# Kernel optimization log

Hardware: AMD Instinct MI355X
Metric: run time of the kernel (lower is better)

The kernel has to match this reference:

```python
import jax, jax.numpy as jnp
import numpy as np

HEAD, STACK = 8, 2
EPS = 1e-5


def _ln2d(x):
    # F.layer_norm(x, x.size()[1:]): normalize over (seq, feature) jointly, no affine
    m = jnp.mean(x, axis=(1, 2), keepdims=True)
    v = jnp.var(x, axis=(1, 2), keepdims=True)
    return (x - m) / jnp.sqrt(v + EPS)


def setup_inputs() -> dict:
    key = jax.random.key(0)
    ks = jax.random.split(key, 8)
    B, S, V, E, D, C = 64, 1024, 8000, 200, 200, 31
    g = lambda k, shape, sc: (jax.random.normal(k, shape, jnp.float32) * sc)
    return dict(
        x=jax.random.randint(ks[0], (B, S), 0, V),
        embed=g(ks[1], (V, E), 0.02),
        pos=g(ks[2], (S, E), 0.02),
        Wp=g(ks[3], (E, D), 0.05), bp=jnp.zeros((D,), jnp.float32),
        Wm=g(ks[4], (D * HEAD, D), 0.05), bm=jnp.zeros((D,), jnp.float32),
        W1=g(ks[5], (D, D), 0.05), b1=jnp.zeros((D,), jnp.float32),
        W2=g(ks[6], (D, D), 0.05), b2=jnp.zeros((D,), jnp.float32),
        Wd=g(ks[7], (D, C), 0.05), bd=jnp.zeros((C,), jnp.float32),
    )


def reference(x, embed, pos, Wp, bp, Wm, bm, W1, b1, W2, b2, Wd, bd):
    h = embed[x] + pos                       # [B,S,200]
    scale = jnp.sqrt(jnp.asarray(Wp.shape[1], jnp.float32))
    for _ in range(STACK):                   # weights shared across stacks (aliased in torch)
        r = h
        p = h @ Wp + bp                      # q = k = v (same aliased Linear in torch)
        a = jax.nn.softmax(jnp.einsum('bsd,btd->bst', p, p) / scale, axis=-1)
        c = jnp.einsum('bst,btd->bsd', a, p)  # [B,S,200]
        cat = jnp.tile(c, (1, 1, HEAD))       # all heads identical -> concat = tile
        h = _ln2d(cat @ Wm + bm + r)
        r = h
        ff = jax.nn.relu(h @ W1 + b1) @ W2 + b2
        h = _ln2d(ff + r)
    return h[:, -1, :] @ Wd + bd             # [B, class_num]; dropout = identity (eval)
```

## Files before the change

### kernel.cpp

```cpp
#include <hip/hip_runtime.h>
#include <cstddef>
#include <cstdint>
#include <cmath>

#define BDIM  64
#define SDIM  1024
#define DDIM  200
#define DPAD  224
#define WROWS 256
#define PSTRIDE 232
#define CDIM  31
#define NSTACK 2
#define EPS   1e-5f
#define LN_N  204800.0f
#define PREP_BLOCKS 224

typedef __attribute__((ext_vector_type(8))) short short8;
typedef __attribute__((ext_vector_type(4))) short short4_t;
typedef __attribute__((ext_vector_type(4))) float f32x4;

__device__ __forceinline__ short f2bf(float f) {
    union { float f; unsigned u; } v; v.f = f;
    unsigned r = v.u + 0x7FFFu + ((v.u >> 16) & 1u);
    return (short)(r >> 16);
}
__device__ __forceinline__ float bf2f(short s) {
    union { unsigned u; float f; } v; v.u = ((unsigned)(unsigned short)s) << 16;
    return v.f;
}
__device__ __forceinline__ unsigned cvtpk_bf16(float a, float b) {
    unsigned r;
    asm volatile("v_cvt_pk_bf16_f32 %0, %1, %2" : "=v"(r) : "v"(a), "v"(b));
    return r;
}
__device__ __forceinline__ void gload_lds16(const short* g, short* l) {
    __builtin_amdgcn_global_load_lds(
        (const __attribute__((address_space(1))) void*)g,
        (__attribute__((address_space(3))) void*)l, 16, 0, 0);
}

__global__ void prep_embed_kernel(const int* __restrict__ x, const float* __restrict__ embed,
                                  const float* __restrict__ pos,
                                  const float* __restrict__ Wp, const float* __restrict__ bp,
                                  const float* __restrict__ Wm, const float* __restrict__ bm,
                                  const float* __restrict__ W1, const float* __restrict__ b1,
                                  const float* __restrict__ W2, const float* __restrict__ b2,
                                  short* __restrict__ WtP, short* __restrict__ WtM,
                                  short* __restrict__ Wt1, short* __restrict__ Wt2,
                                  float* __restrict__ bpP, float* __restrict__ bmP,
                                  float* __restrict__ b1P, float* __restrict__ b2P,
                                  float* __restrict__ csP, float* __restrict__ cs1,
                                  short* __restrict__ h, float* __restrict__ parts)
{
    if (blockIdx.x < PREP_BLOCKS) {
        int idx = blockIdx.x * 256 + threadIdx.x;
        if (idx >= WROWS * DPAD) return;
        int n = idx / DPAD, k = idx - n * DPAD;
        bool valid = (n < DDIM) && (k < DDIM);
        WtP[idx] = valid ? f2bf(Wp[(size_t)k * DDIM + n]) : 0;
        Wt1[idx] = valid ? f2bf(W1[(size_t)k * DDIM + n]) : 0;
        Wt2[idx] = valid ? f2bf(W2[(size_t)k * DDIM + n]) : 0;
        float s = 0.f;
        if (valid) {
            #pragma unroll
            for (int blk = 0; blk < 8; ++blk)
                s += Wm[(size_t)(blk * DDIM + k) * DDIM + n];
        }
        WtM[idx] = valid ? f2bf(s) : 0;
        if (idx < DPAD) {
            bpP[idx] = idx < DDIM ? bp[idx] : 0.f;
            bmP[idx] = idx < DDIM ? bm[idx] : 0.f;
            b1P[idx] = idx < DDIM ? b1[idx] : 0.f;
            b2P[idx] = idx < DDIM ? b2[idx] : 0.f;
            float sp = 0.f, s1 = 0.f;
            if (idx < DDIM) {
                for (int kk = 0; kk < DDIM; ++kk) {
                    sp += bf2f(f2bf(Wp[(size_t)kk * DDIM + idx]));
                    s1 += bf2f(f2bf(W1[(size_t)kk * DDIM + idx]));
                }
            }
            csP[idx] = sp;
            cs1[idx] = s1;
        }
        return;
    }

    const int eb = blockIdx.x - PREP_BLOCKS;
    if (eb == 0) {
        for (int i = threadIdx.x; i < 4 * BDIM * 2; i += 256) parts[i] = 0.f;
    }
    const int total = BDIM * SDIM * (DPAD / 4);
    for (int i = eb * 256 + threadIdx.x; i < total; i += 2048 * 256) {
        const int row = i / (DPAD / 4);
        const int n0  = (i - row * (DPAD / 4)) * 4;
        short4_t o;
        if (n0 >= DDIM) {
            o[0] = o[1] = o[2] = o[3] = 0;
        } else {
            const int s = row & (SDIM - 1);
            const int tok = x[row];
            const float4 e  = *(const float4*)(embed + (size_t)tok * DDIM + n0);
            const float4 p4 = *(const float4*)(pos + (size_t)s * DDIM + n0);
            o[0] = f2bf(e.x + p4.x); o[1] = f2bf(e.y + p4.y);
            o[2] = f2bf(e.z + p4.z); o[3] = f2bf(e.w + p4.w);
        }
        *(short4_t*)(h + (size_t)row * DPAD + n0) = o;
    }
}

#define WSLICE 8192
__global__ __launch_bounds__(256, 3)
void gemm_bf(const short* __restrict__ act, const float* __restrict__ actParts,
             const short* __restrict__ Wt, const float* __restrict__ bias,
             const float* __restrict__ csW,
             const short* __restrict__ res, const float* __restrict__ resParts,
             short* __restrict__ out, short* __restrict__ pt,
             float* __restrict__ parts, int doRelu, int outStride)
{
    __shared__ short WB[3][WSLICE];

    const int tid  = threadIdx.x;
    const int wave = tid >> 6, lane = tid & 63;
    const int lo   = lane & 15, hi = lane >> 4;
    const int mblk = blockIdx.x * 128;
    const int m0   = mblk + wave * 32;

    auto stage = [&](int ks, int buf) {
        #pragma unroll
        for (int cc = 0; cc < 4; ++cc) {
            int c = wave + cc * 4;
            int row = c * 16 + (lane >> 2);
            int kc  = (lane & 3) ^ ((row >> 1) & 3);
            gload_lds16(Wt + (size_t)row * DPAD + ks * 32 + kc * 8,
                        &WB[buf][c * 512 + lane * 8]);
        }
    };

    f32x4 acc[2][14];
    #pragma unroll
    for (int mt = 0; mt < 2; ++mt)
        #pragma unroll
        for (int nt = 0; nt < 14; ++nt) acc[mt][nt] = (f32x4){0.f, 0.f, 0.f, 0.f};

    short8 af[2], afn[2];
    #pragma unroll
    for (int mt = 0; mt < 2; ++mt)
        af[mt] = *(const short8*)(act + (size_t)(m0 + mt * 16 + lo) * DPAD + hi * 8);
    stage(0, 0);
    stage(1, 1);
    asm volatile("s_waitcnt vmcnt(4)" ::: "memory");
    __builtin_amdgcn_s_barrier();

    #pragma unroll
    for (int ks = 0; ks < 7; ++ks) {
        const int cur = ks % 3;
        if (ks < 6) {
            #pragma unroll
            for (int mt = 0; mt < 2; ++mt)
                afn[mt] = *(const short8*)(act + (size_t)(m0 + mt * 16 + lo) * DPAD
                                           + (ks + 1) * 32 + hi * 8);
        }
        if (ks < 5) stage(ks + 2, (ks + 2) % 3);

        #pragma unroll
        for (int nt = 0; nt < 14; ++nt) {
            int brow = nt * 16 + lo;
            short8 bf_ = *(const short8*)&WB[cur][brow * 32
                                                  + ((hi * 8) ^ (((brow >> 1) & 3) << 3))];
            acc[0][nt] = __builtin_amdgcn_mfma_f32_16x16x32_bf16(af[0], bf_, acc[0][nt], 0, 0, 0);
            acc[1][nt] = __builtin_amdgcn_mfma_f32_16x16x32_bf16(af[1], bf_, acc[1][nt], 0, 0, 0);
        }

        if (ks < 5) {
            asm volatile("s_waitcnt vmcnt(6)" ::: "memory");
            __builtin_amdgcn_s_barrier();
        } else if (ks == 5) {
            asm volatile("s_waitcnt vmcnt(2)" ::: "memory");
            __builtin_amdgcn_s_barrier();
        }
        if (ks < 6) { af[0] = afn[0]; af[1] = afn[1]; }
    }

    const int bb = mblk >> 10;
    float inv_a = 1.f, corr = 0.f;
    if (actParts) {
        float mean = actParts[bb * 2] / LN_N;
        inv_a = rsqrtf(actParts[bb * 2 + 1] / LN_N - mean * mean + EPS);
        corr = mean * inv_a;
    }
    float mean_r = 0.f, inv_r = 1.f;
    if (resParts) {
        mean_r = resParts[bb * 2] / LN_N;
        inv_r = rsqrtf(resParts[bb * 2 + 1] / LN_N - mean_r * mean_r + EPS);
    }

    float s = 0.f, s2 = 0.f;
    #pragma unroll
    for (int mt = 0; mt < 2; ++mt) {
        #pragma unroll
        for (int nt = 0; nt < 14; ++nt) {
            const int n = nt * 16 + lo;
            const float bn = bias[n];
            const float cw = actParts ? csW[n] : 0.f;
            float v[4];
            #pragma unroll
            for (int r = 0; r < 4; ++r)
                v[r] = acc[mt][nt][r] * inv_a + bn - corr * cw;
            if (res) {
                #pragma unroll
                for (int r = 0; r < 4; ++r) {
                    int m = m0 + mt * 16 + hi * 4 + r;
                    v[r] += (bf2f(res[(size_t)m * DPAD + n]) - mean_r) * inv_r;
                }
            }
            if (doRelu)
                #pragma unroll
                for (int r = 0; r < 4; ++r) v[r] = fmaxf(v[r], 0.f);
            if (n >= DDIM)
                #pragma unroll
                for (int r = 0; r < 4; ++r) v[r] = 0.f;
            if (parts)
                #pragma unroll
                for (int r = 0; r < 4; ++r) { s += v[r]; s2 = fmaf(v[r], v[r], s2); }
            short4_t o4;
            #pragma unroll
            for (int r = 0; r < 4; ++r) o4[r] = f2bf(v[r]);
            #pragma unroll
            for (int r = 0; r < 4; ++r) {
                int m = m0 + mt * 16 + hi * 4 + r;
                out[(size_t)m * outStride + n] = o4[r];
            }
            if (pt && nt < 13) {
                const int sloc = (m0 + mt * 16 + hi * 4) & (SDIM - 1);
                *(short4_t*)(pt + ((size_t)bb * DPAD + n) * SDIM + sloc) = o4;
            }
        }
    }

    if (parts) {
        __shared__ float rs[4], rq[4];
        #pragma unroll
        for (int off = 32; off; off >>= 1) {
            s  += __shfl_down(s, off);
            s2 += __shfl_down(s2, off);
        }
        if (lane == 0) { rs[wave] = s; rq[wave] = s2; }
        __syncthreads();
        if (tid == 0) {
            atomicAdd(&parts[bb * 2],     rs[0] + rs[1] + rs[2] + rs[3]);
            atomicAdd(&parts[bb * 2 + 1], rq[0] + rq[1] + rq[2] + rq[3]);
        }
    }
}

#define Y1S 232
__global__ __launch_bounds__(256, 2)
void ffn_bf(const short* __restrict__ act, const float* __restrict__ actParts,
            const float* __restrict__ csW1,
            const short* __restrict__ Wt1, const float* __restrict__ b1,
            const short* __restrict__ Wt2, const float* __restrict__ b2,
            short* __restrict__ out, float* __restrict__ parts)
{
    __shared__ short WB[3][WSLICE];
    __shared__ short Y1[64 * Y1S];

    const int tid  = threadIdx.x;
    const int wave = tid >> 6, lane = tid & 63;
    const int lo   = lane & 15, hi = lane >> 4;
    const int mblk = blockIdx.x * 64;
    const int m0   = mblk + wave * 16;
    const int bb   = mblk >> 10;

    auto stageJ = [&](int j) {
        const short* W = (j < 7) ? Wt1 : Wt2;
        const int kk = (j < 7) ? j : j - 7;
        const int buf = j % 3;
        #pragma unroll
        for (int cc = 0; cc < 4; ++cc) {
            int c = wave + cc * 4;
            int row = c * 16 + (lane >> 2);
            int kc  = (lane & 3) ^ ((row >> 1) & 3);
            gload_lds16(W + (size_t)row * DPAD + kk * 32 + kc * 8,
                        &WB[buf][c * 512 + lane * 8]);
        }
    };

    const float mean_a = actParts[bb * 2] / LN_N;
    const float inv_a  = rsqrtf(actParts[bb * 2 + 1] / LN_N - mean_a * mean_a + EPS);
    const float corr   = mean_a * inv_a;

    f32x4 acc[14];
    #pragma unroll
    for (int nt = 0; nt < 14; ++nt) acc[nt] = (f32x4){0.f, 0.f, 0.f, 0.f};

    short8 af = *(const short8*)(act + (size_t)(m0 + lo) * DPAD + hi * 8);
    short8 afn;
    stageJ(0);
    stageJ(1);
    asm volatile("s_waitcnt vmcnt(4)" ::: "memory");
    __builtin_amdgcn_s_barrier();

    #pragma unroll
    for (int ks = 0; ks < 7; ++ks) {
        const int cur = ks % 3;
        if (ks < 6)
            afn = *(const short8*)(act + (size_t)(m0 + lo) * DPAD + (ks + 1) * 32 + hi * 8);
        stageJ(ks + 2);
        #pragma unroll
        for (int nt = 0; nt < 14; ++nt) {
            int brow = nt * 16 + lo;
            short8 bf_ = *(const short8*)&WB[cur][brow * 32
                                                  + ((hi * 8) ^ (((brow >> 1) & 3) << 3))];
            acc[nt] = __builtin_amdgcn_mfma_f32_16x16x32_bf16(af, bf_, acc[nt], 0, 0, 0);
        }
        if (ks < 6) {
            asm volatile("s_waitcnt vmcnt(5)" ::: "memory");
            __builtin_amdgcn_s_barrier();
            af = afn;
        }
    }

    #pragma unroll
    for (int nt = 0; nt < 14; ++nt) {
        const int n = nt * 16 + lo;
        const float bn = b1[n];
        const float cw = csW1[n];
        #pragma unroll
        for (int r = 0; r < 4; ++r) {
            float v = fmaxf(acc[nt][r] * inv_a + bn - corr * cw, 0.f);
            Y1[(wave * 16 + hi * 4 + r) * Y1S + n] = f2bf(v);
        }
    }
    __syncthreads();

    #pragma unroll
    for (int nt = 0; nt < 14; ++nt) acc[nt] = (f32x4){0.f, 0.f, 0.f, 0.f};

    #pragma unroll
    for (int j = 7; j < 14; ++j) {
        const int cur = j % 3;
        if (j < 12) stageJ(j + 2);
        short8 a2 = *(const short8*)&Y1[(wave * 16 + lo) * Y1S + (j - 7) * 32 + hi * 8];
        #pragma unroll
        for (int nt = 0; nt < 14; ++nt) {
            int brow = nt * 16 + lo;
            short8 bf_ = *(const short8*)&WB[cur][brow * 32
                                                  + ((hi * 8) ^ (((brow >> 1) & 3) << 3))];
            acc[nt] = __builtin_amdgcn_mfma_f32_16x16x32_bf16(a2, bf_, acc[nt], 0, 0, 0);
        }
        if (j < 12)       asm volatile("s_waitcnt vmcnt(4)" ::: "memory");
        else if (j == 12) asm volatile("s_waitcnt vmcnt(0)" ::: "memory");
        if (j < 13) __builtin_amdgcn_s_barrier();
    }

    float s = 0.f, s2 = 0.f;
    #pragma unroll
    for (int nt = 0; nt < 14; ++nt) {
        const int n = nt * 16 + lo;
        const float bn = b2[n];
        float v[4];
        #pragma unroll
        for (int r = 0; r < 4; ++r) {
            int m = m0 + hi * 4 + r;
            v[r] = acc[nt][r] + bn + (bf2f(act[(size_t)m * DPAD + n]) - mean_a) * inv_a;
        }
        if (n >= DDIM)
            #pragma unroll
            for (int r = 0; r < 4; ++r) v[r] = 0.f;
        #pragma unroll
        for (int r = 0; r < 4; ++r) { s += v[r]; s2 = fmaf(v[r], v[r], s2); }
        #pragma unroll
        for (int r = 0; r < 4; ++r) {
            int m = m0 + hi * 4 + r;
            out[(size_t)m * DPAD + n] = f2bf(v[r]);
        }
    }

    {
        __shared__ float rs[4], rq[4];
        #pragma unroll
        for (int off = 32; off; off >>= 1) {
            s  += __shfl_down(s, off);
            s2 += __shfl_down(s2, off);
        }
        if (lane == 0) { rs[wave] = s; rq[wave] = s2; }
        __syncthreads();
        if (tid == 0) {
            atomicAdd(&parts[bb * 2],     rs[0] + rs[1] + rs[2] + rs[3]);
            atomicAdd(&parts[bb * 2 + 1], rq[0] + rq[1] + rq[2] + rq[3]);
        }
    }
}

__global__ __launch_bounds__(256, 2)
void attn_kernel(const short* __restrict__ pbf, const short* __restrict__ pt,
                 short* __restrict__ c, float qscale)
{
    __shared__ short Kbuf[2][7680];
    __shared__ short Vbuf[2][6656];

    const int bid = blockIdx.x;
    const int wg  = (bid & 7) * 64 + (bid >> 3);
    const int b   = wg >> 3;
    const int q0  = (wg & 7) * 128;

    const int tid  = threadIdx.x;
    const int wave = tid >> 6;
    const int lane = tid & 63;
    const int lo   = lane & 15;
    const int hi   = lane >> 4;

    const short* pb  = pbf + (size_t)b * SDIM * PSTRIDE;
    const short* ptb = pt  + (size_t)b * DPAD * SDIM;

    auto stage = [&](int kt2, int bufIdx) {
        const short* ks = pb + (size_t)kt2 * 32 * PSTRIDE + lane * 8;
        #pragma unroll
        for (int i = 0; i < 15; ++i)
            gload_lds16(ks + i * 512, &Kbuf[bufIdx][i * 512]);
        #pragma unroll
        for (int i = 0; i < 13; ++i) {
            int e = i * 512 + lane * 8;
            int d = e >> 5;
            int cc = (e & 31) ^ (((d >> 1) & 3) << 3);
            gload_lds16(ptb + (size_t)d * SDIM + kt2 * 32 + cc, &Vbuf[bufIdx][i * 512]);
        }
    };

    short8 qf[2][7];
    #pragma unroll
    for (int qt = 0; qt < 2; ++qt)
        #pragma unroll
        for (int ks = 0; ks < 7; ++ks) {
            short8 q = *(const short8*)(pb + (size_t)(q0 + wave * 32 + qt * 16 + lo) * PSTRIDE
                                        + ks * 32 + hi * 8);
            short8 qs;
            #pragma unroll
            for (int j = 0; j < 8; ++j) qs[j] = f2bf(bf2f(q[j]) * qscale);
            qf[qt][ks] = qs;
        }

    f32x4 o[2][13];
    float m[2], ell[2];
    #pragma unroll
    for (int qt = 0; qt < 2; ++qt) {
        #pragma unroll
        for (int n = 0; n < 13; ++n) o[qt][n] = (f32x4){0.f, 0.f, 0.f, 0.f};
        m[qt] = -1e30f; ell[qt] = 0.f;
    }

    if (wave == 0) stage(0, 0);
    __syncthreads();

    for (int kt = 0; kt < 32; ++kt) {
        const int cur = kt & 1;
        if (kt < 31 && wave == ((kt + 1) & 3)) stage(kt + 1, cur ^ 1);

        f32x4 sacc[2][2];
        #pragma unroll
        for (int qt = 0; qt < 2; ++qt)
            #pragma unroll
            for (int t = 0; t < 2; ++t) sacc[qt][t] = (f32x4){0.f, 0.f, 0.f, 0.f};
        __builtin_amdgcn_s_setprio(1);
        #pragma unroll
        for (int t = 0; t < 2; ++t)
            #pragma unroll
            for (int ks = 0; ks < 7; ++ks) {
                short8 kf = *(const short8*)(&Kbuf[cur][(t * 16 + lo) * PSTRIDE + ks * 32 + hi * 8]);
                sacc[0][t] = __builtin_amdgcn_mfma_f32_16x16x32_bf16(kf, qf[0][ks], sacc[0][t], 0, 0, 0);
                sacc[1][t] = __builtin_amdgcn_mfma_f32_16x16x32_bf16(kf, qf[1][ks], sacc[1][t], 0, 0, 0);
            }
        __builtin_amdgcn_s_setprio(0);

        short8 pa[2];
        #pragma unroll
        for (int qt = 0; qt < 2; ++qt) {
            float mx = fmaxf(fmaxf(fmaxf(sacc[qt][0][0], sacc[qt][0][1]),
                                   fmaxf(sacc[qt][0][2], sacc[qt][0][3])),
                             fmaxf(fmaxf(sacc[qt][1][0], sacc[qt][1][1]),
                                   fmaxf(sacc[qt][1][2], sacc[qt][1][3])));
            mx = fmaxf(mx, __shfl_xor(mx, 16));
            mx = fmaxf(mx, __shfl_xor(mx, 32));
            if (__any(mx > m[qt] + 11.5f)) {
                float mn = fmaxf(m[qt], mx);
                float al = exp2f(m[qt] - mn);
                m[qt] = mn; ell[qt] *= al;
                float alr[4];
                #pragma unroll
                for (int r = 0; r < 4; ++r) alr[r] = __shfl(al, hi * 4 + r);
                #pragma unroll
                for (int n = 0; n < 13; ++n)
                    #pragma unroll
                    for (int r = 0; r < 4; ++r) o[qt][n][r] *= alr[r];
            }
            float p[2][4]; float rsum = 0.f;
            #pragma unroll
            for (int t = 0; t < 2; ++t)
                #pragma unroll
                for (int r = 0; r < 4; ++r) {
                    p[t][r] = exp2f(sacc[qt][t][r] - m[qt]);
                    rsum += p[t][r];
                }
            rsum += __shfl_xor(rsum, 16);
            rsum += __shfl_xor(rsum, 32);
            ell[qt] += rsum;
            unsigned pk01_0 = cvtpk_bf16(p[0][0], p[0][1]);
            unsigned pk23_0 = cvtpk_bf16(p[0][2], p[0][3]);
            unsigned pk01_1 = cvtpk_bf16(p[1][0], p[1][1]);
            unsigned pk23_1 = cvtpk_bf16(p[1][2], p[1][3]);
            const int srcA = lo + ((hi & 1) * 2) * 16;
            const int srcB = srcA + 16;
            int a0 = __shfl((int)pk01_0, srcA), a1 = __shfl((int)pk01_1, srcA);
            int b0 = __shfl((int)pk23_0, srcA), b1 = __shfl((int)pk23_1, srcA);
            int c0 = __shfl((int)pk01_0, srcB), c1 = __shfl((int)pk01_1, srcB);
            int d0 = __shfl((int)pk23_0, srcB), d1 = __shfl((int)pk23_1, srcB);
            const bool thi = (hi >> 1) != 0;
            union { short8 s; int u[4]; } pu;
            pu.u[0] = thi ? a1 : a0;
            pu.u[1] = thi ? b1 : b0;
            pu.u[2] = thi ? c1 : c0;
            pu.u[3] = thi ? d1 : d0;
            pa[qt] = pu.s;
        }

        __builtin_amdgcn_s_setprio(1);
        #pragma unroll
        for (int n = 0; n < 13; ++n) {
            int d = n * 16 + lo;
            int addr = d * 32 + ((hi * 8) ^ (((d >> 1) & 3) << 3));
            short8 vf = *(const short8*)(&Vbuf[cur][addr]);
            o[0][n] = __builtin_amdgcn_mfma_f32_16x16x32_bf16(pa[0], vf, o[0][n], 0, 0, 0);
            o[1][n] = __builtin_amdgcn_mfma_f32_16x16x32_bf16(pa[1], vf, o[1][n], 0, 0, 0);
        }
        __builtin_amdgcn_s_setprio(0);

        __syncthreads();
    }

    #pragma unroll
    for (int qt = 0; qt < 2; ++qt) {
        float inv_l = 1.f / ell[qt];
        float invr[4];
        #pragma unroll
        for (int r = 0; r < 4; ++r) invr[r] = __shfl(inv_l, hi * 4 + r);
        #pragma unroll
        for (int n = 0; n < 13; ++n) {
            int dcol = n * 16 + lo;
            #pragma unroll
            for (int r = 0; r < 4; ++r) {
                size_t row = (size_t)b * SDIM + q0 + wave * 32 + qt * 16 + hi * 4 + r;
                c[row * DPAD + dcol] = f2bf(o[qt][n][r] * invr[r]);
            }
        }
        #pragma unroll
        for (int r = 0; r < 4; ++r) {
            size_t row = (size_t)b * SDIM + q0 + wave * 32 + qt * 16 + hi * 4 + r;
            c[row * DPAD + 208 + lo] = 0;
        }
    }
}

__global__ void final_kernel(const short* __restrict__ y, const float* __restrict__ parts,
                             const float* __restrict__ Wd, const float* __restrict__ bd,
                             float* __restrict__ out)
{
    const int b = blockIdx.x;
    const float sum = parts[b * 2], sq = parts[b * 2 + 1];
    const float mean = sum / LN_N;
    const float inv  = rsqrtf(sq / LN_N - mean * mean + EPS);
    __shared__ float hrow[DDIM];
    const short* row = y + ((size_t)b * SDIM + SDIM - 1) * DPAD;
    for (int d = threadIdx.x; d < DDIM; d += blockDim.x)
        hrow[d] = (bf2f(row[d]) - mean) * inv;
    __syncthreads();
    if (threadIdx.x < CDIM) {
        float acc = bd[threadIdx.x];
        for (int d = 0; d < DDIM; ++d)
            acc = fmaf(hrow[d], Wd[(size_t)d * CDIM + threadIdx.x], acc);
        out[(size_t)b * CDIM + threadIdx.x] = acc;
    }
}

extern "C" void kernel_launch(void* const* d_in, const int* in_sizes, int n_in,
                              void* d_out, int out_size, void* d_ws, size_t ws_size,
                              hipStream_t stream)
{
    const int*   x     = (const int*)  d_in[0];
    const float* embed = (const float*)d_in[1];
    const float* pos   = (const float*)d_in[2];
    const float* Wp    = (const float*)d_in[3];
    const float* bp    = (const float*)d_in[4];
    const float* Wm    = (const float*)d_in[5];
    const float* bm    = (const float*)d_in[6];
    const float* W1    = (const float*)d_in[7];
    const float* b1    = (const float*)d_in[8];
    const float* W2    = (const float*)d_in[9];
    const float* b2    = (const float*)d_in[10];
    const float* Wd    = (const float*)d_in[11];
    const float* bd    = (const float*)d_in[12];
    float* out = (float*)d_out;

    const size_t HB = (size_t)BDIM * SDIM * DPAD;
    const size_t PB = (size_t)BDIM * SDIM * PSTRIDE;
    const size_t WTSZ = (size_t)WROWS * DPAD;

    short* h_bf  = (short*)d_ws;
    short* p_bf  = h_bf  + HB;
    short* pt    = p_bf  + PB;
    short* cb_bf = pt    + HB;
    short* yA    = cb_bf + HB;
    short* yB    = yA    + HB;
    short* WtP   = yB + HB;
    short* WtM   = WtP + WTSZ;
    short* Wt1   = WtM + WTSZ;
    short* Wt2   = Wt1 + WTSZ;
    float* bpP   = (float*)(Wt2 + WTSZ);
    float* bmP   = bpP + DPAD;
    float* b1P   = bmP + DPAD;
    float* b2P   = b1P + DPAD;
    float* csP   = b2P + DPAD;
    float* cs1   = csP + DPAD;
    float* parts = cs1 + DPAD;
    const size_t need = (size_t)((char*)(parts + 4 * BDIM * 2) - (char*)d_ws);
    if (ws_size < need) return;

    float* pA1 = parts;
    float* pB1 = parts + BDIM * 2;
    float* pA2 = parts + 2 * BDIM * 2;
    float* pB2 = parts + 3 * BDIM * 2;

    prep_embed_kernel<<<dim3(PREP_BLOCKS + 2048), dim3(256), 0, stream>>>(
        x, embed, pos, Wp, bp, Wm, bm, W1, b1, W2, b2,
        WtP, WtM, Wt1, Wt2, bpP, bmP, b1P, b2P, csP, cs1, h_bf, parts);

    const float qscale = 1.44269504f / sqrtf((float)DDIM);

    gemm_bf<<<dim3(512), dim3(256), 0, stream>>>(h_bf, nullptr, WtP, bpP, nullptr,
                                                 nullptr, nullptr, p_bf, pt, nullptr, 0, PSTRIDE);
    attn_kernel<<<dim3(512), dim3(256), 0, stream>>>(p_bf, pt, cb_bf, qscale);
    gemm_bf<<<dim3(512), dim3(256), 0, stream>>>(cb_bf, nullptr, WtM, bmP, nullptr,
                                                 h_bf, nullptr, yA, nullptr, pA1, 0, DPAD);
    ffn_bf<<<dim3(1024), dim3(256), 0, stream>>>(yA, pA1, cs1, Wt1, b1P, Wt2, b2P, yB, pB1);
    gemm_bf<<<dim3(512), dim3(256), 0, stream>>>(yB, pB1, WtP, bpP, csP,
                                                 nullptr, nullptr, p_bf, pt, nullptr, 0, PSTRIDE);
    attn_kernel<<<dim3(512), dim3(256), 0, stream>>>(p_bf, pt, cb_bf, qscale);
    gemm_bf<<<dim3(512), dim3(256), 0, stream>>>(cb_bf, nullptr, WtM, bmP, nullptr,
                                                 yB, pB1, h_bf, nullptr, pA2, 0, DPAD);
    ffn_bf<<<dim3(1024), dim3(256), 0, stream>>>(h_bf, pA2, cs1, Wt1, b1P, Wt2, b2P, yA, pB2);
    final_kernel<<<dim3(BDIM), dim3(64), 0, stream>>>(yA, pB2, Wd, bd, out);
}
```

Baseline: 380.3 us.

## Fuse attention with the merge-projection GEMM into one kernel

Attention and the following Wm projection GEMM (with residual, layernorm statistics and atomics) now run in one kernel. Each block writes its attention output rows to global memory, then reuses the same shared memory for triple-buffered Wm slices and runs the GEMM on the rows it just produced. This removes two kernel launches and the separate pass that re-read the attention output. The cost is larger register and LDS pressure in the fused kernel, and the attention output is still written to global memory and read back through cache.

```diff
diff --git a/kernel.cpp b/kernel.cpp
--- a/kernel.cpp
+++ b/kernel.cpp
@@ -14,6 +14,7 @@
 #define EPS   1e-5f
 #define LN_N  204800.0f
 #define PREP_BLOCKS 224
+#define WSLICE 8192
 
 typedef __attribute__((ext_vector_type(8))) short short8;
 typedef __attribute__((ext_vector_type(4))) short short4_t;
@@ -108,14 +109,11 @@
     }
 }
 
-#define WSLICE 8192
 __global__ __launch_bounds__(256, 3)
 void gemm_bf(const short* __restrict__ act, const float* __restrict__ actParts,
              const short* __restrict__ Wt, const float* __restrict__ bias,
              const float* __restrict__ csW,
-             const short* __restrict__ res, const float* __restrict__ resParts,
-             short* __restrict__ out, short* __restrict__ pt,
-             float* __restrict__ parts, int doRelu, int outStride)
+             short* __restrict__ out, short* __restrict__ pt, int outStride)
 {
     __shared__ short WB[3][WSLICE];
 
@@ -188,13 +186,7 @@
         inv_a = rsqrtf(actParts[bb * 2 + 1] / LN_N - mean * mean + EPS);
         corr = mean * inv_a;
     }
-    float mean_r = 0.f, inv_r = 1.f;
-    if (resParts) {
-        mean_r = resParts[bb * 2] / LN_N;
-        inv_r = rsqrtf(resParts[bb * 2 + 1] / LN_N - mean_r * mean_r + EPS);
-    }
-
-    float s = 0.f, s2 = 0.f;
+
     #pragma unroll
     for (int mt = 0; mt < 2; ++mt) {
         #pragma unroll
@@ -206,22 +198,9 @@
             #pragma unroll
             for (int r = 0; r < 4; ++r)
                 v[r] = acc[mt][nt][r] * inv_a + bn - corr * cw;
-            if (res) {
-                #pragma unroll
-                for (int r = 0; r < 4; ++r) {
-                    int m = m0 + mt * 16 + hi * 4 + r;
-                    v[r] += (bf2f(res[(size_t)m * DPAD + n]) - mean_r) * inv_r;
-                }
-            }
-            if (doRelu)
-                #pragma unroll
-                for (int r = 0; r < 4; ++r) v[r] = fmaxf(v[r], 0.f);
             if (n >= DDIM)
                 #pragma unroll
                 for (int r = 0; r < 4; ++r) v[r] = 0.f;
-            if (parts)
-                #pragma unroll
-                for (int r = 0; r < 4; ++r) { s += v[r]; s2 = fmaf(v[r], v[r], s2); }
             short4_t o4;
             #pragma unroll
             for (int r = 0; r < 4; ++r) o4[r] = f2bf(v[r]);
@@ -230,174 +209,27 @@
                 int m = m0 + mt * 16 + hi * 4 + r;
                 out[(size_t)m * outStride + n] = o4[r];
             }
-            if (pt && nt < 13) {
+            if (nt < 13) {
                 const int sloc = (m0 + mt * 16 + hi * 4) & (SDIM - 1);
                 *(short4_t*)(pt + ((size_t)bb * DPAD + n) * SDIM + sloc) = o4;
             }
         }
     }
-
-    if (parts) {
-        __shared__ float rs[4], rq[4];
-        #pragma unroll
-        for (int off = 32; off; off >>= 1) {
-            s  += __shfl_down(s, off);
-            s2 += __shfl_down(s2, off);
-        }
-        if (lane == 0) { rs[wave] = s; rq[wave] = s2; }
-        __syncthreads();
-        if (tid == 0) {
-            atomicAdd(&parts[bb * 2],     rs[0] + rs[1] + rs[2] + rs[3]);
-            atomicAdd(&parts[bb * 2 + 1], rq[0] + rq[1] + rq[2] + rq[3]);
-        }
-    }
-}
-
-#define Y1S 232
+}
+
 __global__ __launch_bounds__(256, 2)
-void ffn_bf(const short* __restrict__ act, const float* __restrict__ actParts,
-            const float* __restrict__ csW1,
-            const short* __restrict__ Wt1, const float* __restrict__ b1,
-            const short* __restrict__ Wt2, const float* __restrict__ b2,
-            short* __restrict__ out, float* __restrict__ parts)
+void attn_gemm2(const short* __restrict__ pbf, const short* __restrict__ pt,
+                const short* __restrict__ WtM, const float* __restrict__ bias,
+                const short* __restrict__ res, const float* __restrict__ resParts,
+                short* __restrict__ cb, short* __restrict__ out,
+                float* __restrict__ parts, float qscale)
 {
-    __shared__ short WB[3][WSLICE];
-    __shared__ short Y1[64 * Y1S];
-
-    const int tid  = threadIdx.x;
-    const int wave = tid >> 6, lane = tid & 63;
-    const int lo   = lane & 15, hi = lane >> 4;
-    const int mblk = blockIdx.x * 64;
-    const int m0   = mblk + wave * 16;
-    const int bb   = mblk >> 10;
-
-    auto stageJ = [&](int j) {
-        const short* W = (j < 7) ? Wt1 : Wt2;
-        const int kk = (j < 7) ? j : j - 7;
-        const int buf = j % 3;
-        #pragma unroll
-        for (int cc = 0; cc < 4; ++cc) {
-            int c = wave + cc * 4;
-            int row = c * 16 + (lane >> 2);
-            int kc  = (lane & 3) ^ ((row >> 1) & 3);
-            gload_lds16(W + (size_t)row * DPAD + kk * 32 + kc * 8,
-                        &WB[buf][c * 512 + lane * 8]);
-        }
-    };
-
-    const float mean_a = actParts[bb * 2] / LN_N;
-    const float inv_a  = rsqrtf(actParts[bb * 2 + 1] / LN_N - mean_a * mean_a + EPS);
-    const float corr   = mean_a * inv_a;
-
-    f32x4 acc[14];
-    #pragma unroll
-    for (int nt = 0; nt < 14; ++nt) acc[nt] = (f32x4){0.f, 0.f, 0.f, 0.f};
-
-    short8 af = *(const short8*)(act + (size_t)(m0 + lo) * DPAD + hi * 8);
-    short8 afn;
-    stageJ(0);
-    stageJ(1);
-    asm volatile("s_waitcnt vmcnt(4)" ::: "memory");
-    __builtin_amdgcn_s_barrier();
-
-    #pragma unroll
-    for (int ks = 0; ks < 7; ++ks) {
-        const int cur = ks % 3;
-        if (ks < 6)
-            afn = *(const short8*)(act + (size_t)(m0 + lo) * DPAD + (ks + 1) * 32 + hi * 8);
-        stageJ(ks + 2);
-        #pragma unroll
-        for (int nt = 0; nt < 14; ++nt) {
-            int brow = nt * 16 + lo;
-            short8 bf_ = *(const short8*)&WB[cur][brow * 32
-                                                  + ((hi * 8) ^ (((brow >> 1) & 3) << 3))];
-            acc[nt] = __builtin_amdgcn_mfma_f32_16x16x32_bf16(af, bf_, acc[nt], 0, 0, 0);
-        }
-        if (ks < 6) {
-            asm volatile("s_waitcnt vmcnt(5)" ::: "memory");
-            __builtin_amdgcn_s_barrier();
-            af = afn;
-        }
-    }
-
-    #pragma unroll
-    for (int nt = 0; nt < 14; ++nt) {
-        const int n = nt * 16 + lo;
-        const float bn = b1[n];
-        const float cw = csW1[n];
-        #pragma unroll
-        for (int r = 0; r < 4; ++r) {
-            float v = fmaxf(acc[nt][r] * inv_a + bn - corr * cw, 0.f);
-            Y1[(wave * 16 + hi * 4 + r) * Y1S + n] = f2bf(v);
-        }
-    }
-    __syncthreads();
-
-    #pragma unroll
-    for (int nt = 0; nt < 14; ++nt) acc[nt] = (f32x4){0.f, 0.f, 0.f, 0.f};
-
-    #pragma unroll
-    for (int j = 7; j < 14; ++j) {
-        const int cur = j % 3;
-        if (j < 12) stageJ(j + 2);
-        short8 a2 = *(const short8*)&Y1[(wave * 16 + lo) * Y1S + (j - 7) * 32 + hi * 8];
-        #pragma unroll
-        for (int nt = 0; nt < 14; ++nt) {
-            int brow = nt * 16 + lo;
-            short8 bf_ = *(const short8*)&WB[cur][brow * 32
-                                                  + ((hi * 8) ^ (((brow >> 1) & 3) << 3))];
-            acc[nt] = __builtin_amdgcn_mfma_f32_16x16x32_bf16(a2, bf_, acc[nt], 0, 0, 0);
-        }
-        if (j < 12)       asm volatile("s_waitcnt vmcnt(4)" ::: "memory");
-        else if (j == 12) asm volatile("s_waitcnt vmcnt(0)" ::: "memory");
-        if (j < 13) __builtin_amdgcn_s_barrier();
-    }
-
-    float s = 0.f, s2 = 0.f;
-    #pragma unroll
-    for (int nt = 0; nt < 14; ++nt) {
-        const int n = nt * 16 + lo;
-        const float bn = b2[n];
-        float v[4];
-        #pragma unroll
-        for (int r = 0; r < 4; ++r) {
-            int m = m0 + hi * 4 + r;
-            v[r] = acc[nt][r] + bn + (bf2f(act[(size_t)m * DPAD + n]) - mean_a) * inv_a;
-        }
-        if (n >= DDIM)
-            #pragma unroll
-            for (int r = 0; r < 4; ++r) v[r] = 0.f;
-        #pragma unroll
-        for (int r = 0; r < 4; ++r) { s += v[r]; s2 = fmaf(v[r], v[r], s2); }
-        #pragma unroll
-        for (int r = 0; r < 4; ++r) {
-            int m = m0 + hi * 4 + r;
-            out[(size_t)m * DPAD + n] = f2bf(v[r]);
-        }
-    }
-
-    {
-        __shared__ float rs[4], rq[4];
-        #pragma unroll
-        for (int off = 32; off; off >>= 1) {
-            s  += __shfl_down(s, off);
-            s2 += __shfl_down(s2, off);
-        }
-        if (lane == 0) { rs[wave] = s; rq[wave] = s2; }
-        __syncthreads();
-        if (tid == 0) {
-            atomicAdd(&parts[bb * 2],     rs[0] + rs[1] + rs[2] + rs[3]);
-            atomicAdd(&parts[bb * 2 + 1], rq[0] + rq[1] + rq[2] + rq[3]);
-        }
-    }
-}
-
-__global__ __launch_bounds__(256, 2)
-void attn_kernel(const short* __restrict__ pbf, const short* __restrict__ pt,
-                 short* __restrict__ c, float qscale)
-{
-    __shared__ short Kbuf[2][7680];
-    __shared__ short Vbuf[2][6656];
+    __shared__ short SH[28672];
+
+    short* Kb0 = SH;
+    short* Kb1 = SH + 7680;
+    short* Vb0 = SH + 15360;
+    short* Vb1 = SH + 22016;
 
     const int bid = blockIdx.x;
     const int wg  = (bid & 7) * 64 + (bid >> 3);
@@ -413,17 +245,19 @@
     const short* pb  = pbf + (size_t)b * SDIM * PSTRIDE;
     const short* ptb = pt  + (size_t)b * DPAD * SDIM;
 
-    auto stage = [&](int kt2, int bufIdx) {
+    auto stageKV = [&](int kt2, int bufIdx) {
+        short* kb = bufIdx ? Kb1 : Kb0;
+        short* vb = bufIdx ? Vb1 : Vb0;
         const short* ks = pb + (size_t)kt2 * 32 * PSTRIDE + lane * 8;
         #pragma unroll
         for (int i = 0; i < 15; ++i)
-            gload_lds16(ks + i * 512, &Kbuf[bufIdx][i * 512]);
+            gload_lds16(ks + i * 512, kb + i * 512);
         #pragma unroll
         for (int i = 0; i < 13; ++i) {
             int e = i * 512 + lane * 8;
             int d = e >> 5;
             int cc = (e & 31) ^ (((d >> 1) & 3) << 3);
-            gload_lds16(ptb + (size_t)d * SDIM + kt2 * 32 + cc, &Vbuf[bufIdx][i * 512]);
+            gload_lds16(ptb + (size_t)d * SDIM + kt2 * 32 + cc, vb + i * 512);
         }
     };
 
@@ -449,12 +283,14 @@
         m[qt] = -1e30f; ell[qt] = 0.f;
     }
 
-    if (wave == 0) stage(0, 0);
+    if (wave == 0) stageKV(0, 0);
     __syncthreads();
 
     for (int kt = 0; kt < 32; ++kt) {
         const int cur = kt & 1;
-        if (kt < 31 && wave == ((kt + 1) & 3)) stage(kt + 1, cur ^ 1);
+        if (kt < 31 && wave == ((kt + 1) & 3)) stageKV(kt + 1, cur ^ 1);
+        const short* kb = cur ? Kb1 : Kb0;
+        const short* vb = cur ? Vb1 : Vb0;
 
         f32x4 sacc[2][2];
         #pragma unroll
@@ -466,7 +302,7 @@
         for (int t = 0; t < 2; ++t)
             #pragma unroll
             for (int ks = 0; ks < 7; ++ks) {
-                short8 kf = *(const short8*)(&Kbuf[cur][(t * 16 + lo) * PSTRIDE + ks * 32 + hi * 8]);
+                short8 kf = *(const short8*)(kb + (t * 16 + lo) * PSTRIDE + ks * 32 + hi * 8);
                 sacc[0][t] = __builtin_amdgcn_mfma_f32_16x16x32_bf16(kf, qf[0][ks], sacc[0][t], 0, 0, 0);
                 sacc[1][t] = __builtin_amdgcn_mfma_f32_16x16x32_bf16(kf, qf[1][ks], sacc[1][t], 0, 0, 0);
             }
@@ -528,7 +364,7 @@
         for (int n = 0; n < 13; ++n) {
             int d = n * 16 + lo;
             int addr = d * 32 + ((hi * 8) ^ (((d >> 1) & 3) << 3));
-            short8 vf = *(const short8*)(&Vbuf[cur][addr]);
+            short8 vf = *(const short8*)(vb + addr);
             o[0][n] = __builtin_amdgcn_mfma_f32_16x16x32_bf16(pa[0], vf, o[0][n], 0, 0, 0);
             o[1][n] = __builtin_amdgcn_mfma_f32_16x16x32_bf16(pa[1], vf, o[1][n], 0, 0, 0);
         }
@@ -549,13 +385,266 @@
             #pragma unroll
             for (int r = 0; r < 4; ++r) {
                 size_t row = (size_t)b * SDIM + q0 + wave * 32 + qt * 16 + hi * 4 + r;
-                c[row * DPAD + dcol] = f2bf(o[qt][n][r] * invr[r]);
+                cb[row * DPAD + dcol] = f2bf(o[qt][n][r] * invr[r]);
             }
         }
         #pragma unroll
         for (int r = 0; r < 4; ++r) {
             size_t row = (size_t)b * SDIM + q0 + wave * 32 + qt * 16 + hi * 4 + r;
-            c[row * DPAD + 208 + lo] = 0;
+            cb[row * DPAD + 208 + lo] = 0;
+        }
+    }
+    asm volatile("s_waitcnt vmcnt(0)" ::: "memory");
+    __builtin_amdgcn_s_barrier();
+
+    short* WB0 = SH;
+    short* WB1 = SH + WSLICE;
+    short* WB2 = SH + 2 * WSLICE;
+
+    const int m0 = b * SDIM + q0 + wave * 32;
+
+    auto stageW = [&](int ks, int buf) {
+        short* wb = (buf == 0) ? WB0 : (buf == 1) ? WB1 : WB2;
+        #pragma unroll
+        for (int cc = 0; cc < 4; ++cc) {
+            int c = wave + cc * 4;
+            int row = c * 16 + (lane >> 2);
+            int kc  = (lane & 3) ^ ((row >> 1) & 3);
+            gload_lds16(WtM + (size_t)row * DPAD + ks * 32 + kc * 8,
+                        wb + c * 512 + lane * 8);
+        }
+    };
+
+    f32x4 acc[2][14];
+    #pragma unroll
+    for (int mt = 0; mt < 2; ++mt)
+        #pragma unroll
+        for (int nt = 0; nt < 14; ++nt) acc[mt][nt] = (f32x4){0.f, 0.f, 0.f, 0.f};
+
+    short8 af[2], afn[2];
+    #pragma unroll
+    for (int mt = 0; mt < 2; ++mt)
+        af[mt] = *(const short8*)(cb + (size_t)(m0 + mt * 16 + lo) * DPAD + hi * 8);
+    stageW(0, 0);
+    stageW(1, 1);
+    asm volatile("s_waitcnt vmcnt(4)" ::: "memory");
+    __builtin_amdgcn_s_barrier();
+
+    #pragma unroll
+    for (int ks = 0; ks < 7; ++ks) {
+        const int cur = ks % 3;
+        short* wb = (cur == 0) ? WB0 : (cur == 1) ? WB1 : WB2;
+        if (ks < 6) {
+            #pragma unroll
+            for (int mt = 0; mt < 2; ++mt)
+                afn[mt] = *(const short8*)(cb + (size_t)(m0 + mt * 16 + lo) * DPAD
+                                           + (ks + 1) * 32 + hi * 8);
+        }
+        if (ks < 5) stageW(ks + 2, (ks + 2) % 3);
+
+        #pragma unroll
+        for (int nt = 0; nt < 14; ++nt) {
+            int brow = nt * 16 + lo;
+            short8 bf_ = *(const short8*)&wb[brow * 32
+                                             + ((hi * 8) ^ (((brow >> 1) & 3) << 3))];
+            acc[0][nt] = __builtin_amdgcn_mfma_f32_16x16x32_bf16(af[0], bf_, acc[0][nt], 0, 0, 0);
+            acc[1][nt] = __builtin_amdgcn_mfma_f32_16x16x32_bf16(af[1], bf_, acc[1][nt], 0, 0, 0);
+        }
+
+        if (ks < 5) {
+            asm volatile("s_waitcnt vmcnt(6)" ::: "memory");
+            __builtin_amdgcn_s_barrier();
+        } else if (ks == 5) {
+            asm volatile("s_waitcnt vmcnt(2)" ::: "memory");
+            __builtin_amdgcn_s_barrier();
+        }
+        if (ks < 6) { af[0] = afn[0]; af[1] = afn[1]; }
+    }
+
+    float mean_r = 0.f, inv_r = 1.f;
+    if (resParts) {
+        mean_r = resParts[b * 2] / LN_N;
+        inv_r = rsqrtf(resParts[b * 2 + 1] / LN_N - mean_r * mean_r + EPS);
+    }
+
+    float s = 0.f, s2 = 0.f;
+    #pragma unroll
+    for (int mt = 0; mt < 2; ++mt) {
+        #pragma unroll
+        for (int nt = 0; nt < 14; ++nt) {
+            const int n = nt * 16 + lo;
+            const float bn = bias[n];
+            float v[4];
+            #pragma unroll
+            for (int r = 0; r < 4; ++r) {
+                int mm = m0 + mt * 16 + hi * 4 + r;
+                v[r] = acc[mt][nt][r] + bn
+                     + (bf2f(res[(size_t)mm * DPAD + n]) - mean_r) * inv_r;
+            }
+            if (n >= DDIM)
+                #pragma unroll
+                for (int r = 0; r < 4; ++r) v[r] = 0.f;
+            #pragma unroll
+            for (int r = 0; r < 4; ++r) { s += v[r]; s2 = fmaf(v[r], v[r], s2); }
+            #pragma unroll
+            for (int r = 0; r < 4; ++r) {
+                int mm = m0 + mt * 16 + hi * 4 + r;
+                out[(size_t)mm * DPAD + n] = f2bf(v[r]);
+            }
+        }
+    }
+
+    {
+        __shared__ float rs[4], rq[4];
+        #pragma unroll
+        for (int off = 32; off; off >>= 1) {
+            s  += __shfl_down(s, off);
+            s2 += __shfl_down(s2, off);
+        }
+        if (lane == 0) { rs[wave] = s; rq[wave] = s2; }
+        __syncthreads();
+        if (tid == 0) {
+            atomicAdd(&parts[b * 2],     rs[0] + rs[1] + rs[2] + rs[3]);
+            atomicAdd(&parts[b * 2 + 1], rq[0] + rq[1] + rq[2] + rq[3]);
+        }
+    }
+}
+
+#define Y1S 232
+__global__ __launch_bounds__(256, 2)
+void ffn_bf(const short* __restrict__ act, const float* __restrict__ actParts,
+            const float* __restrict__ csW1,
+            const short* __restrict__ Wt1, const float* __restrict__ b1,
+            const short* __restrict__ Wt2, const float* __restrict__ b2,
+            short* __restrict__ out, float* __restrict__ parts)
+{
+    __shared__ short WB[3][WSLICE];
+    __shared__ short Y1[64 * Y1S];
+
+    const int tid  = threadIdx.x;
+    const int wave = tid >> 6, lane = tid & 63;
+    const int lo   = lane & 15, hi = lane >> 4;
+    const int mblk = blockIdx.x * 64;
+    const int m0   = mblk + wave * 16;
+    const int bb   = mblk >> 10;
+
+    auto stageJ = [&](int j) {
+        const short* W = (j < 7) ? Wt1 : Wt2;
+        const int kk = (j < 7) ? j : j - 7;
+        const int buf = j % 3;
+        #pragma unroll
+        for (int cc = 0; cc < 4; ++cc) {
+            int c = wave + cc * 4;
+            int row = c * 16 + (lane >> 2);
+            int kc  = (lane & 3) ^ ((row >> 1) & 3);
+            gload_lds16(W + (size_t)row * DPAD + kk * 32 + kc * 8,
+                        &WB[buf][c * 512 + lane * 8]);
+        }
+    };
+
+    const float mean_a = actParts[bb * 2] / LN_N;
+    const float inv_a  = rsqrtf(actParts[bb * 2 + 1] / LN_N - mean_a * mean_a + EPS);
+    const float corr   = mean_a * inv_a;
+
+    f32x4 acc[14];
+    #pragma unroll
+    for (int nt = 0; nt < 14; ++nt) acc[nt] = (f32x4){0.f, 0.f, 0.f, 0.f};
+
+    short8 af = *(const short8*)(act + (size_t)(m0 + lo) * DPAD + hi * 8);
+    short8 afn;
+    stageJ(0);
+    stageJ(1);
+    asm volatile("s_waitcnt vmcnt(4)" ::: "memory");
+    __builtin_amdgcn_s_barrier();
+
+    #pragma unroll
+    for (int ks = 0; ks < 7; ++ks) {
+        const int cur = ks % 3;
+        if (ks < 6)
+            afn = *(const short8*)(act + (size_t)(m0 + lo) * DPAD + (ks + 1) * 32 + hi * 8);
+        stageJ(ks + 2);
+        #pragma unroll
+        for (int nt = 0; nt < 14; ++nt) {
+            int brow = nt * 16 + lo;
+            short8 bf_ = *(const short8*)&WB[cur][brow * 32
+                                                  + ((hi * 8) ^ (((brow >> 1) & 3) << 3))];
+            acc[nt] = __builtin_amdgcn_mfma_f32_16x16x32_bf16(af, bf_, acc[nt], 0, 0, 0);
+        }
+        if (ks < 6) {
+            asm volatile("s_waitcnt vmcnt(5)" ::: "memory");
+            __builtin_amdgcn_s_barrier();
+            af = afn;
+        }
+    }
+
+    #pragma unroll
+    for (int nt = 0; nt < 14; ++nt) {
+        const int n = nt * 16 + lo;
+        const float bn = b1[n];
+        const float cw = csW1[n];
+        #pragma unroll
+        for (int r = 0; r < 4; ++r) {
+            float v = fmaxf(acc[nt][r] * inv_a + bn - corr * cw, 0.f);
+            Y1[(wave * 16 + hi * 4 + r) * Y1S + n] = f2bf(v);
+        }
+    }
+    __syncthreads();
+
+    #pragma unroll
+    for (int nt = 0; nt < 14; ++nt) acc[nt] = (f32x4){0.f, 0.f, 0.f, 0.f};
+
+    #pragma unroll
+    for (int j = 7; j < 14; ++j) {
+        const int cur = j % 3;
+        if (j < 12) stageJ(j + 2);
+        short8 a2 = *(const short8*)&Y1[(wave * 16 + lo) * Y1S + (j - 7) * 32 + hi * 8];
+        #pragma unroll
+        for (int nt = 0; nt < 14; ++nt) {
+            int brow = nt * 16 + lo;
+            short8 bf_ = *(const short8*)&WB[cur][brow * 32
+                                                  + ((hi * 8) ^ (((brow >> 1) & 3) << 3))];
+            acc[nt] = __builtin_amdgcn_mfma_f32_16x16x32_bf16(a2, bf_, acc[nt], 0, 0, 0);
+        }
+        if (j < 12)       asm volatile("s_waitcnt vmcnt(4)" ::: "memory");
+        else if (j == 12) asm volatile("s_waitcnt vmcnt(0)" ::: "memory");
+        if (j < 13) __builtin_amdgcn_s_barrier();
+    }
+
+    float s = 0.f, s2 = 0.f;
+    #pragma unroll
+    for (int nt = 0; nt < 14; ++nt) {
+        const int n = nt * 16 + lo;
+        const float bn = b2[n];
+        float v[4];
+        #pragma unroll
+        for (int r = 0; r < 4; ++r) {
+            int m = m0 + hi * 4 + r;
+            v[r] = acc[nt][r] + bn + (bf2f(act[(size_t)m * DPAD + n]) - mean_a) * inv_a;
+        }
+        if (n >= DDIM)
+            #pragma unroll
+            for (int r = 0; r < 4; ++r) v[r] = 0.f;
+        #pragma unroll
+        for (int r = 0; r < 4; ++r) { s += v[r]; s2 = fmaf(v[r], v[r], s2); }
+        #pragma unroll
+        for (int r = 0; r < 4; ++r) {
+            int m = m0 + hi * 4 + r;
+            out[(size_t)m * DPAD + n] = f2bf(v[r]);
+        }
+    }
+
+    {
+        __shared__ float rs[4], rq[4];
+        #pragma unroll
+        for (int off = 32; off; off >>= 1) {
+            s  += __shfl_down(s, off);
+            s2 += __shfl_down(s2, off);
+        }
+        if (lane == 0) { rs[wave] = s; rq[wave] = s2; }
+        __syncthreads();
+        if (tid == 0) {
+            atomicAdd(&parts[bb * 2],     rs[0] + rs[1] + rs[2] + rs[3]);
+            atomicAdd(&parts[bb * 2 + 1], rq[0] + rq[1] + rq[2] + rq[3]);
         }
     }
 }
@@ -636,16 +725,14 @@
     const float qscale = 1.44269504f / sqrtf((float)DDIM);
 
     gemm_bf<<<dim3(512), dim3(256), 0, stream>>>(h_bf, nullptr, WtP, bpP, nullptr,
-                                                 nullptr, nullptr, p_bf, pt, nullptr, 0, PSTRIDE);
-    attn_kernel<<<dim3(512), dim3(256), 0, stream>>>(p_bf, pt, cb_bf, qscale);
-    gemm_bf<<<dim3(512), dim3(256), 0, stream>>>(cb_bf, nullptr, WtM, bmP, nullptr,
-                                                 h_bf, nullptr, yA, nullptr, pA1, 0, DPAD);
+                                                 p_bf, pt, PSTRIDE);
+    attn_gemm2<<<dim3(512), dim3(256), 0, stream>>>(p_bf, pt, WtM, bmP,
+                                                    h_bf, nullptr, cb_bf, yA, pA1, qscale);
     ffn_bf<<<dim3(1024), dim3(256), 0, stream>>>(yA, pA1, cs1, Wt1, b1P, Wt2, b2P, yB, pB1);
     gemm_bf<<<dim3(512), dim3(256), 0, stream>>>(yB, pB1, WtP, bpP, csP,
-                                                 nullptr, nullptr, p_bf, pt, nullptr, 0, PSTRIDE);
-    attn_kernel<<<dim3(512), dim3(256), 0, stream>>>(p_bf, pt, cb_bf, qscale);
-    gemm_bf<<<dim3(512), dim3(256), 0, stream>>>(cb_bf, nullptr, WtM, bmP, nullptr,
-                                                 yB, pB1, h_bf, nullptr, pA2, 0, DPAD);
+                                                 p_bf, pt, PSTRIDE);
+    attn_gemm2<<<dim3(512), dim3(256), 0, stream>>>(p_bf, pt, WtM, bmP,
+                                                    yB, pB1, cb_bf, h_bf, pA2, qscale);
     ffn_bf<<<dim3(1024), dim3(256), 0, stream>>>(h_bf, pA2, cs1, Wt1, b1P, Wt2, b2P, yA, pB2);
     final_kernel<<<dim3(BDIM), dim3(64), 0, stream>>>(yA, pB2, Wd, bd, out);
 }
```

Result: slower. 389.7 us (+2.4%).
